# Performance work log

Hardware: AMD Instinct MI355X
Metric: run time of the kernel (lower is better)

## Reference

```python
import jax, jax.numpy as jnp
import numpy as np

S, B, D, H = 512, 16, 512, 8  # seq_len, batch, d_model, n_heads
DH = D // H


def setup_inputs() -> dict:
    key = jax.random.key(0)
    k1, k2, k3, k4, k5 = jax.random.split(key, 5)
    x = jax.random.normal(k1, (S, B, D), dtype=jnp.float32)
    # nn.MultiheadAttention params: packed in_proj [3D, D], out_proj [D, D]
    W_in = jax.random.normal(k2, (3 * D, D), dtype=jnp.float32) * (D ** -0.5)
    b_in = jax.random.normal(k3, (3 * D,), dtype=jnp.float32) * 0.02
    W_out = jax.random.normal(k4, (D, D), dtype=jnp.float32) * (D ** -0.5)
    b_out = jax.random.normal(k5, (D,), dtype=jnp.float32) * 0.02
    return {"x": x, "W_in": W_in, "b_in": b_in, "W_out": W_out, "b_out": b_out}


def _mha(q_in, k_in, v_in, W_in, b_in, W_out, b_out):
    """torch.nn.MultiheadAttention (batch_first=False, eval mode). Inputs: (S, B, D)."""
    Wq, Wk, Wv = jnp.split(W_in, 3, axis=0)
    bq, bk, bv = jnp.split(b_in, 3)

    def heads(t):  # (S, B, D) -> (B, H, S, DH)
        s, b, _ = t.shape
        return t.reshape(s, b, H, DH).transpose(1, 2, 0, 3)

    q = heads(q_in @ Wq.T + bq) * (DH ** -0.5)
    k = heads(k_in @ Wk.T + bk)
    v = heads(v_in @ Wv.T + bv)
    attn = jax.nn.softmax(jnp.einsum('bhsd,bhtd->bhst', q, k), axis=-1)
    o = jnp.einsum('bhst,bhtd->bhsd', attn, v)          # (B, H, S, DH)
    o = o.transpose(2, 0, 1, 3).reshape(q_in.shape)      # (S, B, D)
    return o @ W_out.T + b_out


def reference(x, W_in, b_in, W_out, b_out):
    ch = jnp.arange(x.shape[-1])  # channel indices of last dim

    def step(acc, i):
        # x_i: only channel i kept (mirrors x_i[..., i] = x[..., i])
        x_i = jnp.where(ch == i, x, 0.0)
        # x_i_prime = where(x_i == 0, x, 0): x with channel i zeroed (where nonzero)
        x_ip = jnp.where(x_i == 0.0, x, 0.0)
        out = _mha(x_i, x_ip, x_ip, W_in, b_in, W_out, b_out)
        return acc + out, None

    # loop runs x.size(1) times, exactly as the torch code
    acc, _ = jax.lax.scan(step, jnp.zeros_like(x), jnp.arange(x.shape[1]))
    return acc
```

## Files before the change

### kernel.cpp

```cpp
#include <hip/hip_runtime.h>

#define S_LEN 512
#define BATCH 16
#define DMODEL 512
#define NHEAD 8
#define DH 64
#define NI 16

typedef float f32x4 __attribute__((ext_vector_type(4)));
typedef float f32x2 __attribute__((ext_vector_type(2)));
typedef short s16x8 __attribute__((ext_vector_type(8)));

__device__ __forceinline__ unsigned short f2bf(float f){
  unsigned int u = __float_as_uint(f);
  u += 0x7FFFu + ((u >> 16) & 1u);
  return (unsigned short)(u >> 16);
}

__device__ __forceinline__ void async16(const unsigned short* g, unsigned short* l){
  __builtin_amdgcn_global_load_lds(
      (const __attribute__((address_space(1))) unsigned int*)g,
      (__attribute__((address_space(3))) unsigned int*)l, 16, 0, 0);
}

template<int CTRL>
__device__ __forceinline__ float dppAdd(float x){
  int v = __builtin_amdgcn_update_dpp(0, __float_as_int(x), CTRL, 0xF, 0xF, true);
  return x + __int_as_float(v);
}

__device__ __forceinline__ void plswap32(float &a, float &b){
  asm("v_permlane32_swap_b32 %0, %1" : "+v"(a), "+v"(b));
}
__device__ __forceinline__ void plswap16(float &a, float &b){
  asm("v_permlane16_swap_b32 %0, %1" : "+v"(a), "+v"(b));
}
__device__ __forceinline__ unsigned int cvtpk_bf16(float lo, float hi){
  unsigned int r;
  asm("v_cvt_pk_bf16_f32 %0, %1, %2" : "=v"(r) : "v"(lo), "v"(hi));
  return r;
}

__global__ void k_prep(const float* __restrict__ x, unsigned short* __restrict__ xb,
                       float* __restrict__ zcol){
  int tid = blockIdx.x * 256 + threadIdx.x;
  float4 v = reinterpret_cast<const float4*>(x)[tid];
  ushort4 o;
  o.x = f2bf(v.x); o.y = f2bf(v.y); o.z = f2bf(v.z); o.w = f2bf(v.w);
  reinterpret_cast<ushort4*>(xb)[tid] = o;
  int d0 = (tid & 127) * 4;
  if (d0 < 16){
    int row = tid >> 7;
    int t = row >> 4, b = row & 15;
    zcol[(size_t)(b * 16 + d0 + 0) * 512 + t] = v.x;
    zcol[(size_t)(b * 16 + d0 + 1) * 512 + t] = v.y;
    zcol[(size_t)(b * 16 + d0 + 2) * 512 + t] = v.z;
    zcol[(size_t)(b * 16 + d0 + 3) * 512 + t] = v.w;
  }
}

__global__ void k_wcvt(const float* __restrict__ Win, const float* __restrict__ Wout,
                       unsigned short* __restrict__ Winb, unsigned short* __restrict__ Wob){
  int bidx = blockIdx.x;
  if (bidx < 768){
    int t = bidx * 256 + threadIdx.x;
    float4 v = reinterpret_cast<const float4*>(Win)[t];
    ushort4 o;
    o.x = f2bf(v.x); o.y = f2bf(v.y); o.z = f2bf(v.z); o.w = f2bf(v.w);
    reinterpret_cast<ushort4*>(Winb)[t] = o;
  } else {
    int t = (bidx - 768) * 256 + threadIdx.x;
    float4 v = reinterpret_cast<const float4*>(Wout)[t];
    ushort4 o;
    o.x = f2bf(v.x); o.y = f2bf(v.y); o.z = f2bf(v.z); o.w = f2bf(v.w);
    reinterpret_cast<ushort4*>(Wob)[t] = o;
  }
}

__global__ __launch_bounds__(256) void k_kv2(const unsigned short* __restrict__ xb,
    const unsigned short* __restrict__ Winb, const float* __restrict__ b_in,
    float* __restrict__ Kf, unsigned short* __restrict__ Vfb){
  __shared__ unsigned short As[2][128 * 32];
  __shared__ unsigned short Bs[2][128 * 32];
  int tid = threadIdx.x;
  int w = tid >> 6, l = tid & 63;
  int ln = l & 15, kb = l >> 4;
  int wr = w >> 1, wc = w & 1;
  int m0 = blockIdx.x * 128;
  int n0 = blockIdx.y * 128;
  const unsigned short* Brow = Winb + (size_t)512 * DMODEL;

  f32x4 acc[4][4];
  #pragma unroll
  for (int mi = 0; mi < 4; ++mi)
    #pragma unroll
    for (int nj = 0; nj < 4; ++nj) acc[mi][nj] = (f32x4){0.f,0.f,0.f,0.f};

  int c0 = tid, c1 = 256 + tid;
  int r0 = c0 >> 2, q0 = c0 & 3, r1 = c1 >> 2, q1 = c1 & 3;
  int lb0 = (w * 64) * 8, lb1 = (256 + w * 64) * 8;

  #define STAGE_KV(kt, buf) do { int k0 = (kt) * 32;                                   \
    async16(xb   + (size_t)(m0 + r0) * DMODEL + k0 + q0 * 8, &As[buf][lb0]);           \
    async16(xb   + (size_t)(m0 + r1) * DMODEL + k0 + q1 * 8, &As[buf][lb1]);           \
    async16(Brow + (size_t)(n0 + r0) * DMODEL + k0 + q0 * 8, &Bs[buf][lb0]);           \
    async16(Brow + (size_t)(n0 + r1) * DMODEL + k0 + q1 * 8, &Bs[buf][lb1]);           \
  } while(0)

  STAGE_KV(0, 0);
  __syncthreads();
  int cur = 0;
  for (int kt = 0; kt < 16; ++kt){
    if (kt < 15) STAGE_KV(kt + 1, cur ^ 1);
    const unsigned short* Ab = &As[cur][(wr * 64 + ln) * 32 + kb * 8];
    const unsigned short* Bb = &Bs[cur][(wc * 64 + ln) * 32 + kb * 8];
    s16x8 af[4], bf[4];
    #pragma unroll
    for (int mi = 0; mi < 4; ++mi) af[mi] = *reinterpret_cast<const s16x8*>(Ab + mi * 16 * 32);
    #pragma unroll
    for (int nj = 0; nj < 4; ++nj) bf[nj] = *reinterpret_cast<const s16x8*>(Bb + nj * 16 * 32);
    #pragma unroll
    for (int mi = 0; mi < 4; ++mi)
      #pragma unroll
      for (int nj = 0; nj < 4; ++nj)
        acc[mi][nj] = __builtin_amdgcn_mfma_f32_16x16x32_bf16(af[mi], bf[nj], acc[mi][nj], 0, 0, 0);
    __syncthreads();
    cur ^= 1;
  }
  #undef STAGE_KV

  #pragma unroll
  for (int nj = 0; nj < 4; ++nj){
    int n = n0 + wc * 64 + nj * 16 + ln;
    float bias = b_in[512 + n];
    #pragma unroll
    for (int mi = 0; mi < 4; ++mi){
      #pragma unroll
      for (int r = 0; r < 4; ++r){
        int m = m0 + wr * 64 + mi * 16 + kb * 4 + r;
        float v = acc[mi][nj][r] + bias;
        if (n < DMODEL) Kf[(size_t)m * DMODEL + n] = v;
        else            Vfb[(size_t)m * DMODEL + (n - DMODEL)] = f2bf(v);
      }
    }
  }
}

__global__ void k_tr(const unsigned short* __restrict__ Vfb, unsigned short* __restrict__ VfT){
  __shared__ unsigned short tile[32][34];
  int b = blockIdx.z; int t0 = blockIdx.x * 32; int d0 = blockIdx.y * 32;
  int tx = threadIdx.x & 31, ty = threadIdx.x >> 5;
  #pragma unroll
  for (int k = 0; k < 4; ++k){
    int row = ty + 8 * k;
    tile[row][tx] = Vfb[(size_t)((t0 + row) * BATCH + b) * DMODEL + d0 + tx];
  }
  __syncthreads();
  #pragma unroll
  for (int k = 0; k < 4; ++k){
    int row = ty + 8 * k;
    VfT[(size_t)b * (DMODEL * S_LEN) + (size_t)(d0 + row) * S_LEN + t0 + tx] = tile[tx][row];
  }
}

__global__ __launch_bounds__(512) void k_gh(const float* __restrict__ W_in,
    const float* __restrict__ b_in, const float* __restrict__ Kf,
    const float* __restrict__ zcol, float* __restrict__ G, float* __restrict__ H){
  const float SCALE = 0.18033688011112042f;
  int bh = blockIdx.x; int b = bh >> 3, h = bh & 7;
  __shared__ float u[64][17];
  __shared__ float cvec[64];
  __shared__ float alpha[16], beta[16];
  int tid = threadIdx.x;
  for (int idx = tid; idx < 1024; idx += 512){
    int d = idx >> 4, i = idx & 15;
    u[d][i] = W_in[(size_t)(h * 64 + d) * DMODEL + i];
  }
  if (tid < 64) cvec[tid] = b_in[h * 64 + tid];
  __syncthreads();
  if (tid < 16){
    float a = 0.f, be = 0.f;
    for (int d = 0; d < 64; ++d){
      float wk = W_in[(size_t)(512 + h * 64 + d) * DMODEL + tid];
      a  += u[d][tid] * wk;
      be += cvec[d] * wk;
    }
    alpha[tid] = a; beta[tid] = be;
  }
  __syncthreads();
  int t = tid;
  float K[64];
  const float* kp = Kf + (size_t)(t * BATCH + b) * DMODEL + h * 64;
  #pragma unroll
  for (int d = 0; d < 64; d += 4){
    float4 v = *reinterpret_cast<const float4*>(kp + d);
    K[d] = v.x; K[d+1] = v.y; K[d+2] = v.z; K[d+3] = v.w;
  }
  float Bt = 0.f;
  #pragma unroll
  for (int d = 0; d < 64; ++d) Bt += cvec[d] * K[d];
  for (int i = 0; i < 16; ++i){
    float A = 0.f;
    #pragma unroll
    for (int d = 0; d < 64; ++d) A += u[d][i] * K[d];
    float z = zcol[(size_t)(b * 16 + i) * 512 + t];
    G[(size_t)(bh * 16 + i) * 512 + t] = (A  - alpha[i] * z) * SCALE;
    H[(size_t)(bh * 16 + i) * 512 + t] = (Bt - beta[i]  * z) * SCALE;
  }
}

__global__ __launch_bounds__(512) void k_smpv(const float* __restrict__ G,
    const float* __restrict__ H, const float* __restrict__ zcol,
    const unsigned short* __restrict__ VfT, const float* __restrict__ W_in,
    unsigned short* __restrict__ Ob){
  __shared__ unsigned short Pl[32 * 512];
  __shared__ float Rs[32][17];
  __shared__ float Wvl[64][17];
  int j = blockIdx.x;
  int xcd = j & 7, rest = j >> 3;
  int bh_hi = rest & 15, sb = rest >> 4;
  int bh = bh_hi * 8 + xcd;
  int b = bh >> 3, h = bh & 7;
  int tid = threadIdx.x, w = tid >> 6, l = tid & 63;

  for (int idx = tid; idx < 1024; idx += 512){
    int d = idx >> 4, i = idx & 15;
    Wvl[d][i] = W_in[(size_t)(2 * DMODEL + h * 64 + d) * DMODEL + i];
  }

  const float* gb = G    + ((size_t)bh * NI) * S_LEN;
  const float* hb = H    + ((size_t)bh * NI) * S_LEN;
  const float* zb = zcol + ((size_t)b  * NI) * S_LEN;
  int t0 = l * 4, t1 = 256 + l * 4;
  int s_w = sb * 32 + w * 4;

  f32x2 Pacc[4][4];
  #pragma unroll
  for (int r = 0; r < 4; ++r)
    #pragma unroll
    for (int jp = 0; jp < 4; ++jp) Pacc[r][jp] = (f32x2){0.f, 0.f};

  for (int i = 0; i < NI; ++i){
    const float* gp = gb + (i << 9);
    const float* hp = hb + (i << 9);
    const float* zp = zb + (i << 9);
    f32x4 gA = *reinterpret_cast<const f32x4*>(gp + t0);
    f32x4 gB = *reinterpret_cast<const f32x4*>(gp + t1);
    f32x4 hA = *reinterpret_cast<const f32x4*>(hp + t0);
    f32x4 hB = *reinterpret_cast<const f32x4*>(hp + t1);
    f32x4 zA = *reinterpret_cast<const f32x4*>(zp + t0);
    f32x4 zB = *reinterpret_cast<const f32x4*>(zp + t1);
    float4 y4 = *reinterpret_cast<const float4*>(zp + s_w);
    f32x2 g2[4] = {gA.lo, gA.hi, gB.lo, gB.hi};
    f32x2 h2[4] = {hA.lo, hA.hi, hB.lo, hB.hi};
    f32x2 z2[4] = {zA.lo, zA.hi, zB.lo, zB.hi};
    float ys[4] = {y4.x, y4.y, y4.z, y4.w};

    f32x2 E[4][4];
    float pd[4], pr[4];
    #pragma unroll
    for (int r = 0; r < 4; ++r){
      f32x2 yv = {ys[r], ys[r]};
      f32x2 dacc = {0.f, 0.f}, racc = {0.f, 0.f};
      #pragma unroll
      for (int jp = 0; jp < 4; ++jp){
        f32x2 a = yv * g2[jp] + h2[jp];
        f32x2 e;
        e.x = __builtin_amdgcn_exp2f(a.x);
        e.y = __builtin_amdgcn_exp2f(a.y);
        E[r][jp] = e;
        dacc += e;
        racc += e * z2[jp];
      }
      pd[r] = dacc.x + dacc.y;
      pr[r] = racc.x + racc.y;
    }

    plswap32(pd[0], pd[2]);  float dq0 = pd[0] + pd[2];
    plswap32(pd[1], pd[3]);  float dq1 = pd[1] + pd[3];
    plswap32(pr[0], pr[2]);  float rq0 = pr[0] + pr[2];
    plswap32(pr[1], pr[3]);  float rq1 = pr[1] + pr[3];
    plswap16(dq0, dq1);      float du = dq0 + dq1;
    plswap16(rq0, rq1);      float ru = rq0 + rq1;
    du = dppAdd<0x140>(du); ru = dppAdd<0x140>(ru);
    du = dppAdd<0x141>(du); ru = dppAdd<0x141>(ru);
    du = dppAdd<0x4E>(du);  ru = dppAdd<0x4E>(ru);
    du = dppAdd<0xB1>(du);  ru = dppAdd<0xB1>(ru);
    float inv = __builtin_amdgcn_rcpf(du);
    if ((l & 15) == 0)
      Rs[w * 4 + (l >> 4)][i] = ru * inv;
    #pragma unroll
    for (int r = 0; r < 4; ++r){
      float ir = __int_as_float(__builtin_amdgcn_readlane(__float_as_int(inv), 16 * r));
      f32x2 iv = {ir, ir};
      #pragma unroll
      for (int jp = 0; jp < 4; ++jp) Pacc[r][jp] += E[r][jp] * iv;
    }
  }

  #pragma unroll
  for (int r = 0; r < 4; ++r){
    int sl = w * 4 + r;
    unsigned int u0 = cvtpk_bf16(Pacc[r][0].x, Pacc[r][0].y);
    unsigned int u1 = cvtpk_bf16(Pacc[r][1].x, Pacc[r][1].y);
    unsigned int u2 = cvtpk_bf16(Pacc[r][2].x, Pacc[r][2].y);
    unsigned int u3 = cvtpk_bf16(Pacc[r][3].x, Pacc[r][3].y);
    int xr = (sl & 7) << 4;
    char* rowp = (char*)Pl + sl * 1024;
    uint2 v01; v01.x = u0; v01.y = u1;
    uint2 v23; v23.x = u2; v23.y = u3;
    *reinterpret_cast<uint2*>(rowp + ((l * 8) ^ xr)) = v01;
    *reinterpret_cast<uint2*>(rowp + ((512 + l * 8) ^ xr)) = v23;
  }
  __syncthreads();

  int ln = l & 15, kb = l >> 4;
  int sh = (w & 1) * 16;
  int dt = (w >> 1) * 16;
  const unsigned short* bp = VfT + (size_t)b * (DMODEL * S_LEN)
                             + (size_t)(h * 64 + dt + ln) * S_LEN + kb * 8;
  char* arow = (char*)Pl + (sh + ln) * 1024;
  int xa = (ln & 7) << 4;
  f32x4 acc = {0.f, 0.f, 0.f, 0.f};
  #pragma unroll
  for (int kt = 0; kt < 16; ++kt){
    s16x8 af = *reinterpret_cast<const s16x8*>(arow + ((kt * 64 + kb * 16) ^ xa));
    s16x8 bf = *reinterpret_cast<const s16x8*>(bp + kt * 32);
    acc = __builtin_amdgcn_mfma_f32_16x16x32_bf16(af, bf, acc, 0, 0, 0);
  }
  #pragma unroll
  for (int r = 0; r < 4; ++r){
    int sl = sh + kb * 4 + r;
    float corr = 0.f;
    #pragma unroll
    for (int i = 0; i < 16; ++i) corr += Rs[sl][i] * Wvl[dt + ln][i];
    float v = acc[r] - corr;
    int m = sb * 32 + sl;
    Ob[(size_t)(m * BATCH + b) * DMODEL + h * 64 + dt + ln] = f2bf(v);
  }
}

__global__ __launch_bounds__(256) void k_out2(const unsigned short* __restrict__ Ob,
    const unsigned short* __restrict__ Wob, const float* __restrict__ b_out,
    float* __restrict__ out){
  __shared__ unsigned short As[2][128 * 32];
  __shared__ unsigned short Bs[2][128 * 32];
  int tid = threadIdx.x;
  int w = tid >> 6, l = tid & 63;
  int ln = l & 15, kb = l >> 4;
  int wr = w >> 1, wc = w & 1;
  int m0 = blockIdx.x * 128;
  int n0 = blockIdx.y * 128;

  f32x4 acc[4][4];
  #pragma unroll
  for (int mi = 0; mi < 4; ++mi)
    #pragma unroll
    for (int nj = 0; nj < 4; ++nj) acc[mi][nj] = (f32x4){0.f,0.f,0.f,0.f};

  int c0 = tid, c1 = 256 + tid;
  int r0 = c0 >> 2, q0 = c0 & 3, r1 = c1 >> 2, q1 = c1 & 3;
  int lb0 = (w * 64) * 8, lb1 = (256 + w * 64) * 8;

  #define STAGE_O(kt, buf) do { int k0 = (kt) * 32;                                    \
    async16(Ob  + (size_t)(m0 + r0) * DMODEL + k0 + q0 * 8, &As[buf][lb0]);            \
    async16(Ob  + (size_t)(m0 + r1) * DMODEL + k0 + q1 * 8, &As[buf][lb1]);            \
    async16(Wob + (size_t)(n0 + r0) * DMODEL + k0 + q0 * 8, &Bs[buf][lb0]);            \
    async16(Wob + (size_t)(n0 + r1) * DMODEL + k0 + q1 * 8, &Bs[buf][lb1]);            \
  } while(0)

  STAGE_O(0, 0);
  __syncthreads();
  int cur = 0;
  for (int kt = 0; kt < 16; ++kt){
    if (kt < 15) STAGE_O(kt + 1, cur ^ 1);
    const unsigned short* Ab = &As[cur][(wr * 64 + ln) * 32 + kb * 8];
    const unsigned short* Bb = &Bs[cur][(wc * 64 + ln) * 32 + kb * 8];
    s16x8 af[4], bf[4];
    #pragma unroll
    for (int mi = 0; mi < 4; ++mi) af[mi] = *reinterpret_cast<const s16x8*>(Ab + mi * 16 * 32);
    #pragma unroll
    for (int nj = 0; nj < 4; ++nj) bf[nj] = *reinterpret_cast<const s16x8*>(Bb + nj * 16 * 32);
    #pragma unroll
    for (int mi = 0; mi < 4; ++mi)
      #pragma unroll
      for (int nj = 0; nj < 4; ++nj)
        acc[mi][nj] = __builtin_amdgcn_mfma_f32_16x16x32_bf16(af[mi], bf[nj], acc[mi][nj], 0, 0, 0);
    __syncthreads();
    cur ^= 1;
  }
  #undef STAGE_O

  #pragma unroll
  for (int nj = 0; nj < 4; ++nj){
    int n = n0 + wc * 64 + nj * 16 + ln;
    float bias = 16.0f * b_out[n];
    #pragma unroll
    for (int mi = 0; mi < 4; ++mi){
      #pragma unroll
      for (int r = 0; r < 4; ++r){
        int m = m0 + wr * 64 + mi * 16 + kb * 4 + r;
        out[(size_t)m * DMODEL + n] = acc[mi][nj][r] + bias;
      }
    }
  }
}

extern "C" void kernel_launch(void* const* d_in, const int* in_sizes, int n_in,
                              void* d_out, int out_size, void* d_ws, size_t ws_size,
                              hipStream_t stream) {
  const float* x     = (const float*)d_in[0];
  const float* W_in  = (const float*)d_in[1];
  const float* b_in  = (const float*)d_in[2];
  const float* W_out = (const float*)d_in[3];
  const float* b_out = (const float*)d_in[4];
  float* out = (float*)d_out;

  size_t off = 0;
  char* base = (char*)d_ws;
  auto alloc = [&](size_t bytes) -> void* {
    void* p = base + off;
    off += (bytes + 255) & ~(size_t)255;
    return p;
  };
  unsigned short* xb   = (unsigned short*)alloc(8388608);
  unsigned short* Winb = (unsigned short*)alloc(1572864);
  unsigned short* Wob  = (unsigned short*)alloc(524288);
  float*          zcol = (float*)alloc(524288);
  float*          Kf   = (float*)alloc(16777216);
  unsigned short* Vfb  = (unsigned short*)alloc(8388608);
  unsigned short* VfT  = (unsigned short*)alloc(8388608);
  float*          G    = (float*)alloc(4194304);
  float*          H    = (float*)alloc(4194304);
  unsigned short* Ob   = (unsigned short*)alloc(8388608);

  k_prep<<<4096, 256, 0, stream>>>(x, xb, zcol);
  k_wcvt<<<1024, 256, 0, stream>>>(W_in, W_out, Winb, Wob);

  { dim3 g(64, 8); k_kv2<<<g, 256, 0, stream>>>(xb, Winb, b_in, Kf, Vfb); }
  { dim3 g(16, 16, 16); k_tr<<<g, 256, 0, stream>>>(Vfb, VfT); }
  k_gh<<<128, 512, 0, stream>>>(W_in, b_in, Kf, zcol, G, H);

  k_smpv<<<2048, 512, 0, stream>>>(G, H, zcol, VfT, W_in, Ob);

  { dim3 g(64, 4); k_out2<<<g, 256, 0, stream>>>(Ob, Wob, b_out, out); }
}
```

Before: 184.1 us.

## Double-buffer G/H/z rows into LDS via async loads; split k_gh blocks

In k_smpv, the per-iteration G, H and z rows are now staged into a double-buffered LDS array with async global-to-LDS loads, prefetching row i+1 while row i is computed, instead of every wave loading them directly from global memory. A block barrier is added at the end of each iteration. Separately, k_gh is split into 256 blocks of 256 threads instead of 128 blocks of 512 to spread it across more CUs. The trade-off is extra LDS (12 KB), which may lower occupancy, plus a sync per iteration.

```diff
diff --git a/kernel.cpp b/kernel.cpp
--- a/kernel.cpp
+++ b/kernel.cpp
@@ -163,16 +163,17 @@
   }
 }
 
-__global__ __launch_bounds__(512) void k_gh(const float* __restrict__ W_in,
+__global__ __launch_bounds__(256) void k_gh(const float* __restrict__ W_in,
     const float* __restrict__ b_in, const float* __restrict__ Kf,
     const float* __restrict__ zcol, float* __restrict__ G, float* __restrict__ H){
   const float SCALE = 0.18033688011112042f;
-  int bh = blockIdx.x; int b = bh >> 3, h = bh & 7;
+  int bh = blockIdx.x >> 1, th = blockIdx.x & 1;
+  int b = bh >> 3, h = bh & 7;
   __shared__ float u[64][17];
   __shared__ float cvec[64];
   __shared__ float alpha[16], beta[16];
   int tid = threadIdx.x;
-  for (int idx = tid; idx < 1024; idx += 512){
+  for (int idx = tid; idx < 1024; idx += 256){
     int d = idx >> 4, i = idx & 15;
     u[d][i] = W_in[(size_t)(h * 64 + d) * DMODEL + i];
   }
@@ -188,7 +189,7 @@
     alpha[tid] = a; beta[tid] = be;
   }
   __syncthreads();
-  int t = tid;
+  int t = th * 256 + tid;
   float K[64];
   const float* kp = Kf + (size_t)(t * BATCH + b) * DMODEL + h * 64;
   #pragma unroll
@@ -216,6 +217,7 @@
   __shared__ unsigned short Pl[32 * 512];
   __shared__ float Rs[32][17];
   __shared__ float Wvl[64][17];
+  __shared__ float GHZ[2][3][512];
   int j = blockIdx.x;
   int xcd = j & 7, rest = j >> 3;
   int bh_hi = rest & 15, sb = rest >> 4;
@@ -234,23 +236,36 @@
   int t0 = l * 4, t1 = 256 + l * 4;
   int s_w = sb * 32 + w * 4;
 
+  int arr = w >> 1, half = w & 1;
+  const float* sbase = (arr == 0 ? gb : (arr == 1 ? hb : zb)) + half * 256;
+
   f32x2 Pacc[4][4];
   #pragma unroll
   for (int r = 0; r < 4; ++r)
     #pragma unroll
     for (int jp = 0; jp < 4; ++jp) Pacc[r][jp] = (f32x2){0.f, 0.f};
 
+  if (w < 6)
+    async16((const unsigned short*)sbase + (size_t)l * 8,
+            (unsigned short*)&GHZ[0][arr][half * 256]);
+  __syncthreads();
+
   for (int i = 0; i < NI; ++i){
-    const float* gp = gb + (i << 9);
-    const float* hp = hb + (i << 9);
-    const float* zp = zb + (i << 9);
-    f32x4 gA = *reinterpret_cast<const f32x4*>(gp + t0);
-    f32x4 gB = *reinterpret_cast<const f32x4*>(gp + t1);
-    f32x4 hA = *reinterpret_cast<const f32x4*>(hp + t0);
-    f32x4 hB = *reinterpret_cast<const f32x4*>(hp + t1);
-    f32x4 zA = *reinterpret_cast<const f32x4*>(zp + t0);
-    f32x4 zB = *reinterpret_cast<const f32x4*>(zp + t1);
-    float4 y4 = *reinterpret_cast<const float4*>(zp + s_w);
+    int cb = i & 1;
+    if (i + 1 < NI && w < 6)
+      async16((const unsigned short*)(sbase + ((i + 1) << 9)) + (size_t)l * 8,
+              (unsigned short*)&GHZ[cb ^ 1][arr][half * 256]);
+
+    const float* Gl = &GHZ[cb][0][0];
+    const float* Hl = &GHZ[cb][1][0];
+    const float* Zl = &GHZ[cb][2][0];
+    f32x4 gA = *reinterpret_cast<const f32x4*>(Gl + t0);
+    f32x4 gB = *reinterpret_cast<const f32x4*>(Gl + t1);
+    f32x4 hA = *reinterpret_cast<const f32x4*>(Hl + t0);
+    f32x4 hB = *reinterpret_cast<const f32x4*>(Hl + t1);
+    f32x4 zA = *reinterpret_cast<const f32x4*>(Zl + t0);
+    f32x4 zB = *reinterpret_cast<const f32x4*>(Zl + t1);
+    float4 y4 = *reinterpret_cast<const float4*>(Zl + s_w);
     f32x2 g2[4] = {gA.lo, gA.hi, gB.lo, gB.hi};
     f32x2 h2[4] = {hA.lo, hA.hi, hB.lo, hB.hi};
     f32x2 z2[4] = {zA.lo, zA.hi, zB.lo, zB.hi};
@@ -296,6 +311,7 @@
       #pragma unroll
       for (int jp = 0; jp < 4; ++jp) Pacc[r][jp] += E[r][jp] * iv;
     }
+    __syncthreads();
   }
 
   #pragma unroll
@@ -439,7 +455,7 @@
 
   { dim3 g(64, 8); k_kv2<<<g, 256, 0, stream>>>(xb, Winb, b_in, Kf, Vfb); }
   { dim3 g(16, 16, 16); k_tr<<<g, 256, 0, stream>>>(Vfb, VfT); }
-  k_gh<<<128, 512, 0, stream>>>(W_in, b_in, Kf, zcol, G, H);
+  k_gh<<<256, 256, 0, stream>>>(W_in, b_in, Kf, zcol, G, H);
 
   k_smpv<<<2048, 512, 0, stream>>>(G, H, zcol, VfT, W_in, Ob);
 
```

Measured after the change: 187.2 us. No clear change (+1.7%).
